# Optimization experiments

Hardware: AMD Instinct MI355X
Metric: run time of the kernel (lower is better)

## Reference

```python
import jax, jax.numpy as jnp
import numpy as np

GROUPS = 32
EPS = 1e-6

def group_norm(x, gamma, beta):
    b, c, h, w = x.shape
    xg = x.reshape(b, GROUPS, c // GROUPS, h, w)
    mu = jnp.mean(xg, axis=(2, 3, 4), keepdims=True)
    var = jnp.var(xg, axis=(2, 3, 4), keepdims=True)
    xn = ((xg - mu) * jax.lax.rsqrt(var + EPS)).reshape(b, c, h, w)
    return xn * gamma[None, :, None, None] + beta[None, :, None, None]

def conv1x1(x, w, b):
    # 1x1 conv == channel matmul: [B,C,H,W] x [O,C] -> [B,O,H,W]
    return jnp.einsum('bchw,oc->bohw', x, w) + b[None, :, None, None]

def setup_inputs() -> dict:
    key = jax.random.key(0)
    ks = jax.random.split(key, 5)
    B, C, H, W = 4, 512, 64, 64
    s = 1.0 / np.sqrt(C)
    return {
        'x': jax.random.normal(ks[0], (B, C, H, W), jnp.float32),
        'gn_gamma': jnp.ones((C,), jnp.float32),
        'gn_beta': jnp.zeros((C,), jnp.float32),
        'wq': jax.random.normal(ks[1], (C, C), jnp.float32) * s,
        'bq': jnp.zeros((C,), jnp.float32),
        'wk': jax.random.normal(ks[2], (C, C), jnp.float32) * s,
        'bk': jnp.zeros((C,), jnp.float32),
        'wv': jax.random.normal(ks[3], (C, C), jnp.float32) * s,
        'bv': jnp.zeros((C,), jnp.float32),
        'wp': jax.random.normal(ks[4], (C, C), jnp.float32) * s,
        'bp': jnp.zeros((C,), jnp.float32),
    }

def reference(x, gn_gamma, gn_beta, wq, bq, wk, bk, wv, bv, wp, bp):
    b, c, h, w = x.shape
    h_ = group_norm(x, gn_gamma, gn_beta)
    q = conv1x1(h_, wq, bq).reshape(b, c, h * w)  # [B,C,N]
    k = conv1x1(h_, wk, bk).reshape(b, c, h * w)
    v = conv1x1(h_, wv, bv).reshape(b, c, h * w)
    scale = jnp.asarray(c, x.dtype) ** -0.5
    # scores[b,i,j] = sum_c q[b,c,i] * k[b,c,j]
    scores = jnp.einsum('bci,bcj->bij', q, k) * scale
    attn = jax.nn.softmax(scores, axis=-1)  # softmax over keys j
    # out[b,c,i] = sum_j v[b,c,j] * attn[b,i,j]
    out = jnp.einsum('bcj,bij->bci', v, attn).reshape(b, c, h, w)
    out = conv1x1(out, wp, bp)
    return x + out
```

## Files before the change

### kernel.cpp

```cpp
#include <hip/hip_runtime.h>
#include <stdint.h>

#define B_N 4
#define C_N 512
#define SP_N 4096
#define NG 32
#define CPG 16
#define EPS_ 1e-6f

using bf16x8 = __attribute__((ext_vector_type(8))) __bf16;
using f32x4  = __attribute__((ext_vector_type(4))) float;

#define MFMA16(a, b, c) __builtin_amdgcn_mfma_f32_16x16x32_bf16(a, b, c, 0, 0, 0)

#define GLOAD16(gsrc, ldst) \
    __builtin_amdgcn_global_load_lds( \
        (const __attribute__((address_space(1))) unsigned int*)(gsrc), \
        (__attribute__((address_space(3))) unsigned int*)(ldst), 16, 0, 0)

__device__ __forceinline__ unsigned short f2bf(float f) {
    union { float f; unsigned u; } v; v.f = f;
    unsigned r = v.u + 0x7FFFu + ((v.u >> 16) & 1u);
    return (unsigned short)(r >> 16);
}
__device__ __forceinline__ float bf2f(unsigned short s) {
    union { unsigned u; float f; } v; v.u = ((unsigned)s) << 16;
    return v.f;
}

__global__ void wconv(const float* __restrict__ a, const float* __restrict__ b,
                      const float* __restrict__ c, const float* __restrict__ d,
                      unsigned short* __restrict__ dst) {
    int m = blockIdx.y;
    const float* src = m == 0 ? a : m == 1 ? b : m == 2 ? c : d;
    int i = blockIdx.x * 256 + threadIdx.x;
    float4 v = ((const float4*)src)[i];
    ushort4 o;
    o.x = f2bf(v.x); o.y = f2bf(v.y); o.z = f2bf(v.z); o.w = f2bf(v.w);
    ((ushort4*)(dst + (size_t)m * 262144))[i] = o;
}

__global__ __launch_bounds__(512) void gn_kernel(const float* __restrict__ x,
        const float* __restrict__ gamma, const float* __restrict__ beta,
        unsigned short* __restrict__ h_t) {
    int blk = blockIdx.x;
    int b = blk >> 5, g = blk & 31;
    const float* xg = x + ((size_t)(b * C_N + g * CPG)) * SP_N;
    int t = threadIdx.x;

    float s = 0.f, ss = 0.f;
    const float4* xv = (const float4*)xg;
    for (int i = t; i < (CPG * SP_N) / 4; i += 512) {
        float4 v = xv[i];
        s  += v.x + v.y + v.z + v.w;
        ss += v.x * v.x + v.y * v.y + v.z * v.z + v.w * v.w;
    }
    for (int m = 32; m; m >>= 1) { s += __shfl_xor(s, m); ss += __shfl_xor(ss, m); }
    __shared__ float rs[8], rss[8], stats[2];
    int wid = t >> 6;
    if ((t & 63) == 0) { rs[wid] = s; rss[wid] = ss; }
    __syncthreads();
    if (t == 0) {
        float a = 0.f, q = 0.f;
        for (int i = 0; i < 8; i++) { a += rs[i]; q += rss[i]; }
        float mean = a / (float)(CPG * SP_N);
        float var  = q / (float)(CPG * SP_N) - mean * mean;
        stats[0] = mean;
        stats[1] = rsqrtf(var + EPS_);
    }
    __shared__ float gam[CPG], bet[CPG];
    if (t < CPG) { gam[t] = gamma[g * CPG + t]; bet[t] = beta[g * CPG + t]; }
    __syncthreads();
    float mean = stats[0], rstd = stats[1];

    __shared__ unsigned short tile[CPG][130];
    unsigned short* hb = h_t + (size_t)b * SP_N * C_N;
    for (int n0 = 0; n0 < SP_N; n0 += 128) {
        __syncthreads();
#pragma unroll
        for (int p = 0; p < 4; p++) {
            int cc = p * 4 + (t >> 7);
            int nn = t & 127;
            float v = xg[(size_t)cc * SP_N + n0 + nn];
            v = (v - mean) * rstd * gam[cc] + bet[cc];
            tile[cc][nn] = f2bf(v);
        }
        __syncthreads();
#pragma unroll
        for (int p = 0; p < 4; p++) {
            int idx = p * 512 + t;
            int cc = idx & 15, nn = idx >> 4;
            hb[(size_t)(n0 + nn) * C_N + g * CPG + cc] = tile[cc][nn];
        }
    }
}

template<int MODE>
__global__ __launch_bounds__(256) void gemm_nt(
        const unsigned short* __restrict__ Ab,
        const unsigned short* __restrict__ Bb,
        void* __restrict__ outp,
        const float* __restrict__ bias,
        const float* __restrict__ resid,
        float qs) {
    __shared__ unsigned short at[128 * 64], bt[128 * 64];
    const int z = blockIdx.z;
    const size_t boff = (size_t)z * SP_N * C_N;
    const unsigned short* A;
    const unsigned short* Bm;
    int ldo;
    if (MODE <= 1) { A = Ab + boff; Bm = Bb; ldo = C_N; }
    else           { A = Ab;        Bm = Bb + boff; ldo = SP_N; }
    const int m0 = blockIdx.x * 128, n0 = blockIdx.y * 128;
    const int t = threadIdx.x;
    const int w = t >> 6, l = t & 63;
    const int wr = w >> 1, wc = w & 1;
    const int g = l >> 4, lr = l & 15;

    const f32x4 fz = {0.f, 0.f, 0.f, 0.f};
    f32x4 acc[4][4];
#pragma unroll
    for (int i = 0; i < 4; i++)
#pragma unroll
        for (int j = 0; j < 4; j++) acc[i][j] = fz;

    for (int k0 = 0; k0 < 512; k0 += 64) {
        __syncthreads();
#pragma unroll
        for (int r = 0; r < 4; r++) {
            int chunk = r * 256 + t;
            int row = chunk >> 3, ck = chunk & 7;
            uint4 da = *(const uint4*)(A + (size_t)(m0 + row) * 512 + k0 + ck * 8);
            *(uint4*)((char*)at + row * 128 + ((ck ^ (row & 7)) * 16)) = da;
            uint4 db = *(const uint4*)(Bm + (size_t)(n0 + row) * 512 + k0 + ck * 8);
            *(uint4*)((char*)bt + row * 128 + ((ck ^ (row & 7)) * 16)) = db;
        }
        __syncthreads();
#pragma unroll
        for (int ks = 0; ks < 2; ks++) {
            bf16x8 af[4], bfr[4];
#pragma unroll
            for (int mi = 0; mi < 4; mi++) {
                int row = wr * 64 + mi * 16 + lr;
                af[mi] = *(const bf16x8*)((const char*)at + row * 128 + (((ks * 4 + g) ^ (row & 7)) * 16));
            }
#pragma unroll
            for (int ni = 0; ni < 4; ni++) {
                int row = wc * 64 + ni * 16 + lr;
                bfr[ni] = *(const bf16x8*)((const char*)bt + row * 128 + (((ks * 4 + g) ^ (row & 7)) * 16));
            }
#pragma unroll
            for (int mi = 0; mi < 4; mi++)
#pragma unroll
                for (int ni = 0; ni < 4; ni++)
                    acc[mi][ni] = MFMA16(af[mi], bfr[ni], acc[mi][ni]);
        }
    }
#pragma unroll
    for (int mi = 0; mi < 4; mi++) {
#pragma unroll
        for (int ni = 0; ni < 4; ni++) {
            int col  = n0 + wc * 64 + ni * 16 + lr;
            int rowb = m0 + wr * 64 + mi * 16 + g * 4;
#pragma unroll
            for (int r = 0; r < 4; r++) {
                int row = rowb + r;
                float vv = acc[mi][ni][r];
                if (MODE == 0) {
                    size_t oi = boff + (size_t)row * ldo + col;
                    vv = (vv + bias[col]) * qs;
                    ((unsigned short*)outp)[oi] = f2bf(vv);
                } else if (MODE == 1) {
                    size_t oi = boff + (size_t)row * ldo + col;
                    vv += bias[col];
                    ((unsigned short*)outp)[oi] = f2bf(vv);
                } else if (MODE == 2) {
                    size_t oi = boff + (size_t)(col >> 5) * (C_N * 32) + row * 32 + (col & 31);
                    vv += bias[row];
                    ((unsigned short*)outp)[oi] = f2bf(vv);
                } else {
                    size_t oi = boff + (size_t)row * ldo + col;
                    vv += bias[row] + resid[oi];
                    ((float*)outp)[oi] = vv;
                }
            }
        }
    }
}

__global__ __launch_bounds__(256, 2) void attn_kernel(
        const unsigned short* __restrict__ qt,
        const unsigned short* __restrict__ kt,
        const unsigned short* __restrict__ vm,
        unsigned short* __restrict__ o0,
        unsigned short* __restrict__ o1,
        float* __restrict__ marr,
        float* __restrict__ larr) {
    __shared__ unsigned short k_lds[32 * 512];
    __shared__ unsigned short v_lds[512 * 40];
    __shared__ unsigned short p_lds[4][16 * 32];

    const int bid = blockIdx.x;
    const int bs = bid & 7;
    const int qtile = bid >> 3;
    const int b = bs >> 1;
    const int s = bs & 1;
    const int t = threadIdx.x;
    const int w = t >> 6;
    const int l = t & 63;
    const int g = l >> 4;
    const int lr = l & 15;

    unsigned short* outp = s == 0 ? o0 : o1;
    const int j_beg = s * (SP_N / 2);

    const unsigned short* qb = qt + ((size_t)b * SP_N + qtile * 64 + w * 16) * C_N;
    const unsigned short* kb = kt + (size_t)b * SP_N * C_N;
    const unsigned short* vb = vm + (size_t)b * SP_N * C_N;

    bf16x8 qf[16];
#pragma unroll
    for (int ks = 0; ks < 16; ks++)
        qf[ks] = *(const bf16x8*)(qb + (size_t)lr * C_N + ks * 32 + g * 8);

    const f32x4 fz = {0.f, 0.f, 0.f, 0.f};
    f32x4 oacc[32];
#pragma unroll
    for (int i = 0; i < 32; i++) oacc[i] = fz;
    f32x4 mst = {-1e30f, -1e30f, -1e30f, -1e30f};
    f32x4 lst = {0.f, 0.f, 0.f, 0.f};

    for (int j0 = j_beg; j0 < j_beg + SP_N / 2; j0 += 32) {
        __syncthreads();

#pragma unroll
        for (int r = 0; r < 8; r++) {
            int row = w * 8 + r;
            const unsigned short* src = kb + (size_t)(j0 + row) * C_N + (l ^ (row & 7)) * 8;
            GLOAD16(src, (char*)k_lds + row * 1024);
        }
        const unsigned short* vt = vb + (size_t)(j0 >> 5) * (C_N * 32);
        uint4 vdat[8];
#pragma unroll
        for (int r = 0; r < 8; r++) {
            int chunk = r * 256 + t;
            vdat[r] = *(const uint4*)(vt + (size_t)chunk * 8);
        }
#pragma unroll
        for (int r = 0; r < 8; r++) {
            int chunk = r * 256 + t;
            int c = chunk >> 2, jc = chunk & 3;
            *(uint4*)((char*)v_lds + c * 80 + jc * 16) = vdat[r];
        }
        __syncthreads();

        f32x4 s0 = fz, s1 = fz;
#pragma unroll
        for (int ks = 0; ks < 16; ks++) {
            bf16x8 kf0 = *(const bf16x8*)((const char*)k_lds + lr * 1024 + (((ks * 4 + g) ^ (lr & 7)) * 16));
            s0 = MFMA16(qf[ks], kf0, s0);
            int row1 = 16 + lr;
            bf16x8 kf1 = *(const bf16x8*)((const char*)k_lds + row1 * 1024 + (((ks * 4 + g) ^ (row1 & 7)) * 16));
            s1 = MFMA16(qf[ks], kf1, s1);
        }
        f32x4 mt;
#pragma unroll
        for (int r = 0; r < 4; r++) mt[r] = fmaxf(s0[r], s1[r]);
#pragma unroll
        for (int msk = 1; msk <= 8; msk <<= 1) {
#pragma unroll
            for (int r = 0; r < 4; r++) mt[r] = fmaxf(mt[r], __shfl_xor(mt[r], msk));
        }
        int inc = (mt[0] > mst[0]) || (mt[1] > mst[1]) || (mt[2] > mst[2]) || (mt[3] > mst[3]);
        if (__any(inc)) {
            f32x4 alpha;
#pragma unroll
            for (int r = 0; r < 4; r++) {
                float mn = fmaxf(mst[r], mt[r]);
                alpha[r] = exp2f(mst[r] - mn);
                mst[r] = mn;
                lst[r] *= alpha[r];
            }
            int src = (lr >> 2) << 4;
            float a0 = __shfl(alpha[0], src), a1 = __shfl(alpha[1], src);
            float a2 = __shfl(alpha[2], src), a3 = __shfl(alpha[3], src);
            int rr = lr & 3;
            float ac = rr == 0 ? a0 : rr == 1 ? a1 : rr == 2 ? a2 : a3;
#pragma unroll
            for (int i = 0; i < 32; i++) {
#pragma unroll
                for (int r = 0; r < 4; r++) oacc[i][r] *= ac;
            }
        }
        f32x4 p0, p1, rsum;
#pragma unroll
        for (int r = 0; r < 4; r++) {
            p0[r] = exp2f(s0[r] - mst[r]);
            p1[r] = exp2f(s1[r] - mst[r]);
            rsum[r] = p0[r] + p1[r];
        }
#pragma unroll
        for (int msk = 1; msk <= 8; msk <<= 1) {
#pragma unroll
            for (int r = 0; r < 4; r++) rsum[r] += __shfl_xor(rsum[r], msk);
        }
#pragma unroll
        for (int r = 0; r < 4; r++) lst[r] += rsum[r];

#pragma unroll
        for (int r = 0; r < 4; r++) {
            int i = g * 4 + r;
            int ja = lr;
            *(unsigned short*)((char*)p_lds[w] + i * 64 + (((ja >> 3) ^ ((i >> 1) & 3)) * 16) + (ja & 7) * 2) = f2bf(p0[r]);
            int jb = 16 + lr;
            *(unsigned short*)((char*)p_lds[w] + i * 64 + (((jb >> 3) ^ ((i >> 1) & 3)) * 16) + (jb & 7) * 2) = f2bf(p1[r]);
        }
        bf16x8 pf = *(const bf16x8*)((const char*)p_lds[w] + lr * 64 + ((g ^ ((lr >> 1) & 3)) * 16));
#pragma unroll
        for (int ct = 0; ct < 32; ct++) {
            int row = ct * 16 + lr;
            bf16x8 vf = *(const bf16x8*)((const char*)v_lds + row * 80 + g * 16);
            oacc[ct] = MFMA16(vf, pf, oacc[ct]);
        }
    }

    unsigned short* aob = outp + ((size_t)b * SP_N + qtile * 64 + w * 16 + lr) * C_N;
#pragma unroll
    for (int ct = 0; ct < 32; ct++) {
        int c0 = ct * 16 + g * 4;
        ushort4 o4;
        o4.x = f2bf(oacc[ct][0]);
        o4.y = f2bf(oacc[ct][1]);
        o4.z = f2bf(oacc[ct][2]);
        o4.w = f2bf(oacc[ct][3]);
        *(ushort4*)(aob + c0) = o4;
    }
    if (lr == 0) {
        int base = (s * B_N + b) * SP_N + qtile * 64 + w * 16 + g * 4;
#pragma unroll
        for (int r = 0; r < 4; r++) {
            marr[base + r] = mst[r];
            larr[base + r] = lst[r];
        }
    }
}

__global__ __launch_bounds__(256) void attn_combine(
        const unsigned short* __restrict__ o0,
        const unsigned short* __restrict__ o1,
        const float* __restrict__ marr,
        const float* __restrict__ larr,
        unsigned short* __restrict__ ao) {
    const int w = threadIdx.x >> 6, l = threadIdx.x & 63;
    const size_t row = (size_t)blockIdx.x * 4 + w;
    float m0 = marr[row], m1 = marr[B_N * SP_N + row];
    float l0 = larr[row], l1 = larr[B_N * SP_N + row];
    float m = fmaxf(m0, m1);
    float w0 = exp2f(m0 - m), w1 = exp2f(m1 - m);
    float den = w0 * l0 + w1 * l1;
    float a0 = w0 / den, a1 = w1 / den;
    uint4 u0 = *(const uint4*)(o0 + row * C_N + l * 8);
    uint4 u1 = *(const uint4*)(o1 + row * C_N + l * 8);
    const unsigned short* s0p = (const unsigned short*)&u0;
    const unsigned short* s1p = (const unsigned short*)&u1;
    unsigned short r8[8];
#pragma unroll
    for (int i = 0; i < 8; i++)
        r8[i] = f2bf(a0 * bf2f(s0p[i]) + a1 * bf2f(s1p[i]));
    *(uint4*)(ao + row * C_N + l * 8) = *(const uint4*)r8;
}

extern "C" void kernel_launch(void* const* d_in, const int* in_sizes, int n_in,
                              void* d_out, int out_size, void* d_ws, size_t ws_size,
                              hipStream_t stream) {
    const float* x   = (const float*)d_in[0];
    const float* gam = (const float*)d_in[1];
    const float* bet = (const float*)d_in[2];
    const float* wq  = (const float*)d_in[3];
    const float* bq  = (const float*)d_in[4];
    const float* wk  = (const float*)d_in[5];
    const float* bk  = (const float*)d_in[6];
    const float* wv  = (const float*)d_in[7];
    const float* bv  = (const float*)d_in[8];
    const float* wp  = (const float*)d_in[9];
    const float* bp  = (const float*)d_in[10];

    char* ws = (char*)d_ws;
    const size_t SZ = (size_t)B_N * SP_N * C_N * 2;
    unsigned short* h_t = (unsigned short*)(ws);
    unsigned short* q_t = (unsigned short*)(ws + SZ);
    unsigned short* k_t = (unsigned short*)(ws + 2 * SZ);
    unsigned short* v_m = (unsigned short*)(ws + 3 * SZ);
    unsigned short* wbf = (unsigned short*)(ws + 4 * SZ);
    unsigned short* wq_b = wbf;
    unsigned short* wk_b = wbf + 262144;
    unsigned short* wv_b = wbf + 2 * 262144;
    unsigned short* wp_b = wbf + 3 * 262144;
    float* marr = (float*)(ws + 4 * SZ + 4 * 524288);
    float* larr = marr + 2 * B_N * SP_N;

    unsigned short* o0 = h_t;
    unsigned short* o1 = (unsigned short*)d_out;
    unsigned short* ao = q_t;

    const float qs = 0.044194173824159216f * 1.4426950408889634f;

    wconv<<<dim3(256, 4), 256, 0, stream>>>(wq, wk, wv, wp, wbf);
    gn_kernel<<<dim3(128), 512, 0, stream>>>(x, gam, bet, h_t);
    gemm_nt<0><<<dim3(32, 4, 4), 256, 0, stream>>>(h_t, wq_b, q_t, bq, nullptr, qs);
    gemm_nt<1><<<dim3(32, 4, 4), 256, 0, stream>>>(h_t, wk_b, k_t, bk, nullptr, 1.f);
    gemm_nt<2><<<dim3(4, 32, 4), 256, 0, stream>>>(wv_b, h_t, v_m, bv, nullptr, 1.f);
    attn_kernel<<<dim3(512), 256, 0, stream>>>(q_t, k_t, v_m, o0, o1, marr, larr);
    attn_combine<<<dim3(B_N * SP_N / 4), 256, 0, stream>>>(o0, o1, marr, larr, ao);
    gemm_nt<3><<<dim3(4, 32, 4), 256, 0, stream>>>(wp_b, ao, d_out, bp, x, 1.f);
}
```

Before: 703.4 us.

## Split attention keys three ways and read V directly from global memory

The key range is now split into three parts instead of two, so the grid has 768 blocks and a third partial output buffer. The combine kernel merges three partial softmax states. V is no longer staged through shared memory; each lane loads its V fragments straight from global memory. Dropping the V tile frees LDS, which lets the launch bound ask for 3 blocks per CU. The trade-off is uncached, uncoalesced-per-MFMA global V reads and extra combine traffic.

```diff
diff --git a/kernel.cpp b/kernel.cpp
--- a/kernel.cpp
+++ b/kernel.cpp
@@ -7,6 +7,7 @@
 #define NG 32
 #define CPG 16
 #define EPS_ 1e-6f
+#define NSPLIT 3
 
 using bf16x8 = __attribute__((ext_vector_type(8))) __bf16;
 using f32x4  = __attribute__((ext_vector_type(4))) float;
@@ -188,31 +189,32 @@
     }
 }
 
-__global__ __launch_bounds__(256, 2) void attn_kernel(
+__global__ __launch_bounds__(256, 3) void attn_kernel(
         const unsigned short* __restrict__ qt,
         const unsigned short* __restrict__ kt,
         const unsigned short* __restrict__ vm,
         unsigned short* __restrict__ o0,
         unsigned short* __restrict__ o1,
+        unsigned short* __restrict__ o2,
         float* __restrict__ marr,
         float* __restrict__ larr) {
     __shared__ unsigned short k_lds[32 * 512];
-    __shared__ unsigned short v_lds[512 * 40];
     __shared__ unsigned short p_lds[4][16 * 32];
 
     const int bid = blockIdx.x;
-    const int bs = bid & 7;
-    const int qtile = bid >> 3;
-    const int b = bs >> 1;
-    const int s = bs & 1;
+    const int sb = bid % 12;
+    const int qtile = bid / 12;
+    const int b = sb & 3;
+    const int s = sb >> 2;
     const int t = threadIdx.x;
     const int w = t >> 6;
     const int l = t & 63;
     const int g = l >> 4;
     const int lr = l & 15;
 
-    unsigned short* outp = s == 0 ? o0 : o1;
-    const int j_beg = s * (SP_N / 2);
+    unsigned short* outp = s == 0 ? o0 : (s == 1 ? o1 : o2);
+    const int jt_beg = s * 43;
+    const int jt_end = (s == 2) ? 128 : (s + 1) * 43;
 
     const unsigned short* qb = qt + ((size_t)b * SP_N + qtile * 64 + w * 16) * C_N;
     const unsigned short* kb = kt + (size_t)b * SP_N * C_N;
@@ -230,7 +232,8 @@
     f32x4 mst = {-1e30f, -1e30f, -1e30f, -1e30f};
     f32x4 lst = {0.f, 0.f, 0.f, 0.f};
 
-    for (int j0 = j_beg; j0 < j_beg + SP_N / 2; j0 += 32) {
+    for (int jt = jt_beg; jt < jt_end; jt++) {
+        const int j0 = jt * 32;
         __syncthreads();
 
 #pragma unroll
@@ -238,19 +241,6 @@
             int row = w * 8 + r;
             const unsigned short* src = kb + (size_t)(j0 + row) * C_N + (l ^ (row & 7)) * 8;
             GLOAD16(src, (char*)k_lds + row * 1024);
-        }
-        const unsigned short* vt = vb + (size_t)(j0 >> 5) * (C_N * 32);
-        uint4 vdat[8];
-#pragma unroll
-        for (int r = 0; r < 8; r++) {
-            int chunk = r * 256 + t;
-            vdat[r] = *(const uint4*)(vt + (size_t)chunk * 8);
-        }
-#pragma unroll
-        for (int r = 0; r < 8; r++) {
-            int chunk = r * 256 + t;
-            int c = chunk >> 2, jc = chunk & 3;
-            *(uint4*)((char*)v_lds + c * 80 + jc * 16) = vdat[r];
         }
         __syncthreads();
 
@@ -316,10 +306,11 @@
             *(unsigned short*)((char*)p_lds[w] + i * 64 + (((jb >> 3) ^ ((i >> 1) & 3)) * 16) + (jb & 7) * 2) = f2bf(p1[r]);
         }
         bf16x8 pf = *(const bf16x8*)((const char*)p_lds[w] + lr * 64 + ((g ^ ((lr >> 1) & 3)) * 16));
+
+        const unsigned short* vt = vb + (size_t)jt * (C_N * 32);
 #pragma unroll
         for (int ct = 0; ct < 32; ct++) {
-            int row = ct * 16 + lr;
-            bf16x8 vf = *(const bf16x8*)((const char*)v_lds + row * 80 + g * 16);
+            bf16x8 vf = *(const bf16x8*)(vt + (ct * 16 + lr) * 32 + g * 8);
             oacc[ct] = MFMA16(vf, pf, oacc[ct]);
         }
     }
@@ -348,25 +339,28 @@
 __global__ __launch_bounds__(256) void attn_combine(
         const unsigned short* __restrict__ o0,
         const unsigned short* __restrict__ o1,
+        const unsigned short* __restrict__ o2,
         const float* __restrict__ marr,
         const float* __restrict__ larr,
         unsigned short* __restrict__ ao) {
     const int w = threadIdx.x >> 6, l = threadIdx.x & 63;
     const size_t row = (size_t)blockIdx.x * 4 + w;
-    float m0 = marr[row], m1 = marr[B_N * SP_N + row];
-    float l0 = larr[row], l1 = larr[B_N * SP_N + row];
-    float m = fmaxf(m0, m1);
-    float w0 = exp2f(m0 - m), w1 = exp2f(m1 - m);
-    float den = w0 * l0 + w1 * l1;
-    float a0 = w0 / den, a1 = w1 / den;
+    float m0 = marr[row], m1 = marr[B_N * SP_N + row], m2 = marr[2 * B_N * SP_N + row];
+    float l0 = larr[row], l1 = larr[B_N * SP_N + row], l2 = larr[2 * B_N * SP_N + row];
+    float m = fmaxf(fmaxf(m0, m1), m2);
+    float w0 = exp2f(m0 - m), w1 = exp2f(m1 - m), w2 = exp2f(m2 - m);
+    float den = w0 * l0 + w1 * l1 + w2 * l2;
+    float a0 = w0 / den, a1 = w1 / den, a2 = w2 / den;
     uint4 u0 = *(const uint4*)(o0 + row * C_N + l * 8);
     uint4 u1 = *(const uint4*)(o1 + row * C_N + l * 8);
+    uint4 u2 = *(const uint4*)(o2 + row * C_N + l * 8);
     const unsigned short* s0p = (const unsigned short*)&u0;
     const unsigned short* s1p = (const unsigned short*)&u1;
+    const unsigned short* s2p = (const unsigned short*)&u2;
     unsigned short r8[8];
 #pragma unroll
     for (int i = 0; i < 8; i++)
-        r8[i] = f2bf(a0 * bf2f(s0p[i]) + a1 * bf2f(s1p[i]));
+        r8[i] = f2bf(a0 * bf2f(s0p[i]) + a1 * bf2f(s1p[i]) + a2 * bf2f(s2p[i]));
     *(uint4*)(ao + row * C_N + l * 8) = *(const uint4*)r8;
 }
 
@@ -397,10 +391,11 @@
     unsigned short* wv_b = wbf + 2 * 262144;
     unsigned short* wp_b = wbf + 3 * 262144;
     float* marr = (float*)(ws + 4 * SZ + 4 * 524288);
-    float* larr = marr + 2 * B_N * SP_N;
+    float* larr = marr + NSPLIT * B_N * SP_N;
 
     unsigned short* o0 = h_t;
     unsigned short* o1 = (unsigned short*)d_out;
+    unsigned short* o2 = (unsigned short*)d_out + (size_t)B_N * SP_N * C_N;
     unsigned short* ao = q_t;
 
     const float qs = 0.044194173824159216f * 1.4426950408889634f;
@@ -410,7 +405,7 @@
     gemm_nt<0><<<dim3(32, 4, 4), 256, 0, stream>>>(h_t, wq_b, q_t, bq, nullptr, qs);
     gemm_nt<1><<<dim3(32, 4, 4), 256, 0, stream>>>(h_t, wk_b, k_t, bk, nullptr, 1.f);
     gemm_nt<2><<<dim3(4, 32, 4), 256, 0, stream>>>(wv_b, h_t, v_m, bv, nullptr, 1.f);
-    attn_kernel<<<dim3(512), 256, 0, stream>>>(q_t, k_t, v_m, o0, o1, marr, larr);
-    attn_combine<<<dim3(B_N * SP_N / 4), 256, 0, stream>>>(o0, o1, marr, larr, ao);
+    attn_kernel<<<dim3(768), 256, 0, stream>>>(q_t, k_t, v_m, o0, o1, o2, marr, larr);
+    attn_combine<<<dim3(B_N * SP_N / 4), 256, 0, stream>>>(o0, o1, o2, marr, larr, ao);
     gemm_nt<3><<<dim3(4, 32, 4), 256, 0, stream>>>(wp_b, ao, d_out, bp, x, 1.f);
 }
```

New measurement: 1.186 ms. 1.69x slower.

## Process two query sub-tiles per wave in attention to reuse K/V LDS loads

Applied to the files above, without the earlier changes.

Each wave now handles 32 query rows (two 16-row sub-tiles) instead of 16, so each K and V tile staged in LDS feeds twice as many MFMAs. The grid is halved to 256 blocks and launch bounds drop to one block per CU to make room for the doubled accumulators and Q fragments. The V staging load is also split into two halves to limit live registers. The trade-off is fewer waves in flight, so less latency hiding, and only 256 blocks, which may underfill the GPU's compute units.

```diff
diff --git a/kernel.cpp b/kernel.cpp
--- a/kernel.cpp
+++ b/kernel.cpp
@@ -188,7 +188,7 @@
     }
 }
 
-__global__ __launch_bounds__(256, 2) void attn_kernel(
+__global__ __launch_bounds__(256, 1) void attn_kernel(
         const unsigned short* __restrict__ qt,
         const unsigned short* __restrict__ kt,
         const unsigned short* __restrict__ vm,
@@ -198,7 +198,7 @@
         float* __restrict__ larr) {
     __shared__ unsigned short k_lds[32 * 512];
     __shared__ unsigned short v_lds[512 * 40];
-    __shared__ unsigned short p_lds[4][16 * 32];
+    __shared__ unsigned short p_lds[4][2][16 * 32];
 
     const int bid = blockIdx.x;
     const int bs = bid & 7;
@@ -214,21 +214,25 @@
     unsigned short* outp = s == 0 ? o0 : o1;
     const int j_beg = s * (SP_N / 2);
 
-    const unsigned short* qb = qt + ((size_t)b * SP_N + qtile * 64 + w * 16) * C_N;
+    const unsigned short* qb = qt + ((size_t)b * SP_N + qtile * 128 + w * 32) * C_N;
     const unsigned short* kb = kt + (size_t)b * SP_N * C_N;
     const unsigned short* vb = vm + (size_t)b * SP_N * C_N;
 
-    bf16x8 qf[16];
-#pragma unroll
-    for (int ks = 0; ks < 16; ks++)
-        qf[ks] = *(const bf16x8*)(qb + (size_t)lr * C_N + ks * 32 + g * 8);
+    bf16x8 qf[2][16];
+#pragma unroll
+    for (int sub = 0; sub < 2; sub++)
+#pragma unroll
+        for (int ks = 0; ks < 16; ks++)
+            qf[sub][ks] = *(const bf16x8*)(qb + (size_t)(sub * 16 + lr) * C_N + ks * 32 + g * 8);
 
     const f32x4 fz = {0.f, 0.f, 0.f, 0.f};
-    f32x4 oacc[32];
-#pragma unroll
-    for (int i = 0; i < 32; i++) oacc[i] = fz;
-    f32x4 mst = {-1e30f, -1e30f, -1e30f, -1e30f};
-    f32x4 lst = {0.f, 0.f, 0.f, 0.f};
+    f32x4 oacc[2][32];
+#pragma unroll
+    for (int sub = 0; sub < 2; sub++)
+#pragma unroll
+        for (int i = 0; i < 32; i++) oacc[sub][i] = fz;
+    f32x4 mst[2] = {{-1e30f, -1e30f, -1e30f, -1e30f}, {-1e30f, -1e30f, -1e30f, -1e30f}};
+    f32x4 lst[2] = {fz, fz};
 
     for (int j0 = j_beg; j0 < j_beg + SP_N / 2; j0 += 32) {
         __syncthreads();
@@ -240,107 +244,128 @@
             GLOAD16(src, (char*)k_lds + row * 1024);
         }
         const unsigned short* vt = vb + (size_t)(j0 >> 5) * (C_N * 32);
-        uint4 vdat[8];
-#pragma unroll
-        for (int r = 0; r < 8; r++) {
-            int chunk = r * 256 + t;
-            vdat[r] = *(const uint4*)(vt + (size_t)chunk * 8);
-        }
-#pragma unroll
-        for (int r = 0; r < 8; r++) {
-            int chunk = r * 256 + t;
-            int c = chunk >> 2, jc = chunk & 3;
-            *(uint4*)((char*)v_lds + c * 80 + jc * 16) = vdat[r];
-        }
-        __syncthreads();
-
-        f32x4 s0 = fz, s1 = fz;
+        {
+            uint4 vdat[4];
+#pragma unroll
+            for (int r = 0; r < 4; r++) vdat[r] = *(const uint4*)(vt + (size_t)(r * 256 + t) * 8);
+#pragma unroll
+            for (int r = 0; r < 4; r++) {
+                int chunk = r * 256 + t;
+                *(uint4*)((char*)v_lds + (chunk >> 2) * 80 + (chunk & 3) * 16) = vdat[r];
+            }
+#pragma unroll
+            for (int r = 0; r < 4; r++) vdat[r] = *(const uint4*)(vt + (size_t)((r + 4) * 256 + t) * 8);
+#pragma unroll
+            for (int r = 0; r < 4; r++) {
+                int chunk = (r + 4) * 256 + t;
+                *(uint4*)((char*)v_lds + (chunk >> 2) * 80 + (chunk & 3) * 16) = vdat[r];
+            }
+        }
+        __syncthreads();
+
+        f32x4 s00 = fz, s01 = fz, s10 = fz, s11 = fz;
 #pragma unroll
         for (int ks = 0; ks < 16; ks++) {
             bf16x8 kf0 = *(const bf16x8*)((const char*)k_lds + lr * 1024 + (((ks * 4 + g) ^ (lr & 7)) * 16));
-            s0 = MFMA16(qf[ks], kf0, s0);
             int row1 = 16 + lr;
             bf16x8 kf1 = *(const bf16x8*)((const char*)k_lds + row1 * 1024 + (((ks * 4 + g) ^ (row1 & 7)) * 16));
-            s1 = MFMA16(qf[ks], kf1, s1);
-        }
-        f32x4 mt;
-#pragma unroll
-        for (int r = 0; r < 4; r++) mt[r] = fmaxf(s0[r], s1[r]);
-#pragma unroll
-        for (int msk = 1; msk <= 8; msk <<= 1) {
-#pragma unroll
-            for (int r = 0; r < 4; r++) mt[r] = fmaxf(mt[r], __shfl_xor(mt[r], msk));
-        }
-        int inc = (mt[0] > mst[0]) || (mt[1] > mst[1]) || (mt[2] > mst[2]) || (mt[3] > mst[3]);
-        if (__any(inc)) {
-            f32x4 alpha;
-#pragma unroll
-            for (int r = 0; r < 4; r++) {
-                float mn = fmaxf(mst[r], mt[r]);
-                alpha[r] = exp2f(mst[r] - mn);
-                mst[r] = mn;
-                lst[r] *= alpha[r];
-            }
-            int src = (lr >> 2) << 4;
-            float a0 = __shfl(alpha[0], src), a1 = __shfl(alpha[1], src);
-            float a2 = __shfl(alpha[2], src), a3 = __shfl(alpha[3], src);
-            int rr = lr & 3;
-            float ac = rr == 0 ? a0 : rr == 1 ? a1 : rr == 2 ? a2 : a3;
-#pragma unroll
-            for (int i = 0; i < 32; i++) {
-#pragma unroll
-                for (int r = 0; r < 4; r++) oacc[i][r] *= ac;
-            }
-        }
-        f32x4 p0, p1, rsum;
-#pragma unroll
-        for (int r = 0; r < 4; r++) {
-            p0[r] = exp2f(s0[r] - mst[r]);
-            p1[r] = exp2f(s1[r] - mst[r]);
-            rsum[r] = p0[r] + p1[r];
-        }
-#pragma unroll
-        for (int msk = 1; msk <= 8; msk <<= 1) {
-#pragma unroll
-            for (int r = 0; r < 4; r++) rsum[r] += __shfl_xor(rsum[r], msk);
-        }
-#pragma unroll
-        for (int r = 0; r < 4; r++) lst[r] += rsum[r];
-
-#pragma unroll
-        for (int r = 0; r < 4; r++) {
-            int i = g * 4 + r;
-            int ja = lr;
-            *(unsigned short*)((char*)p_lds[w] + i * 64 + (((ja >> 3) ^ ((i >> 1) & 3)) * 16) + (ja & 7) * 2) = f2bf(p0[r]);
-            int jb = 16 + lr;
-            *(unsigned short*)((char*)p_lds[w] + i * 64 + (((jb >> 3) ^ ((i >> 1) & 3)) * 16) + (jb & 7) * 2) = f2bf(p1[r]);
-        }
-        bf16x8 pf = *(const bf16x8*)((const char*)p_lds[w] + lr * 64 + ((g ^ ((lr >> 1) & 3)) * 16));
+            s00 = MFMA16(qf[0][ks], kf0, s00);
+            s01 = MFMA16(qf[0][ks], kf1, s01);
+            s10 = MFMA16(qf[1][ks], kf0, s10);
+            s11 = MFMA16(qf[1][ks], kf1, s11);
+        }
+
+        bf16x8 pf[2];
+#pragma unroll
+        for (int sub = 0; sub < 2; sub++) {
+            f32x4 sA = sub == 0 ? s00 : s10;
+            f32x4 sB = sub == 0 ? s01 : s11;
+            f32x4 mt;
+#pragma unroll
+            for (int r = 0; r < 4; r++) mt[r] = fmaxf(sA[r], sB[r]);
+#pragma unroll
+            for (int msk = 1; msk <= 8; msk <<= 1) {
+#pragma unroll
+                for (int r = 0; r < 4; r++) mt[r] = fmaxf(mt[r], __shfl_xor(mt[r], msk));
+            }
+            int inc = (mt[0] > mst[sub][0]) || (mt[1] > mst[sub][1]) ||
+                      (mt[2] > mst[sub][2]) || (mt[3] > mst[sub][3]);
+            if (__any(inc)) {
+                f32x4 alpha;
+#pragma unroll
+                for (int r = 0; r < 4; r++) {
+                    float mn = fmaxf(mst[sub][r], mt[r]);
+                    alpha[r] = exp2f(mst[sub][r] - mn);
+                    mst[sub][r] = mn;
+                    lst[sub][r] *= alpha[r];
+                }
+                int src = (lr >> 2) << 4;
+                float a0 = __shfl(alpha[0], src), a1 = __shfl(alpha[1], src);
+                float a2 = __shfl(alpha[2], src), a3 = __shfl(alpha[3], src);
+                int rr = lr & 3;
+                float ac = rr == 0 ? a0 : rr == 1 ? a1 : rr == 2 ? a2 : a3;
+#pragma unroll
+                for (int i = 0; i < 32; i++) {
+#pragma unroll
+                    for (int r = 0; r < 4; r++) oacc[sub][i][r] *= ac;
+                }
+            }
+            f32x4 p0, p1, rsum;
+#pragma unroll
+            for (int r = 0; r < 4; r++) {
+                p0[r] = exp2f(sA[r] - mst[sub][r]);
+                p1[r] = exp2f(sB[r] - mst[sub][r]);
+                rsum[r] = p0[r] + p1[r];
+            }
+#pragma unroll
+            for (int msk = 1; msk <= 8; msk <<= 1) {
+#pragma unroll
+                for (int r = 0; r < 4; r++) rsum[r] += __shfl_xor(rsum[r], msk);
+            }
+#pragma unroll
+            for (int r = 0; r < 4; r++) lst[sub][r] += rsum[r];
+
+            char* pb = (char*)p_lds + (w * 2 + sub) * 1024;
+#pragma unroll
+            for (int r = 0; r < 4; r++) {
+                int i = g * 4 + r;
+                int ja = lr;
+                *(unsigned short*)(pb + i * 64 + (((ja >> 3) ^ ((i >> 1) & 3)) * 16) + (ja & 7) * 2) = f2bf(p0[r]);
+                int jb = 16 + lr;
+                *(unsigned short*)(pb + i * 64 + (((jb >> 3) ^ ((i >> 1) & 3)) * 16) + (jb & 7) * 2) = f2bf(p1[r]);
+            }
+            pf[sub] = *(const bf16x8*)(pb + lr * 64 + ((g ^ ((lr >> 1) & 3)) * 16));
+        }
+
 #pragma unroll
         for (int ct = 0; ct < 32; ct++) {
             int row = ct * 16 + lr;
             bf16x8 vf = *(const bf16x8*)((const char*)v_lds + row * 80 + g * 16);
-            oacc[ct] = MFMA16(vf, pf, oacc[ct]);
-        }
-    }
-
-    unsigned short* aob = outp + ((size_t)b * SP_N + qtile * 64 + w * 16 + lr) * C_N;
-#pragma unroll
-    for (int ct = 0; ct < 32; ct++) {
-        int c0 = ct * 16 + g * 4;
-        ushort4 o4;
-        o4.x = f2bf(oacc[ct][0]);
-        o4.y = f2bf(oacc[ct][1]);
-        o4.z = f2bf(oacc[ct][2]);
-        o4.w = f2bf(oacc[ct][3]);
-        *(ushort4*)(aob + c0) = o4;
-    }
-    if (lr == 0) {
-        int base = (s * B_N + b) * SP_N + qtile * 64 + w * 16 + g * 4;
-#pragma unroll
-        for (int r = 0; r < 4; r++) {
-            marr[base + r] = mst[r];
-            larr[base + r] = lst[r];
+            oacc[0][ct] = MFMA16(vf, pf[0], oacc[0][ct]);
+            oacc[1][ct] = MFMA16(vf, pf[1], oacc[1][ct]);
+        }
+    }
+
+#pragma unroll
+    for (int sub = 0; sub < 2; sub++) {
+        unsigned short* aob = outp + ((size_t)b * SP_N + qtile * 128 + w * 32 + sub * 16 + lr) * C_N;
+#pragma unroll
+        for (int ct = 0; ct < 32; ct++) {
+            int c0 = ct * 16 + g * 4;
+            ushort4 o4;
+            o4.x = f2bf(oacc[sub][ct][0]);
+            o4.y = f2bf(oacc[sub][ct][1]);
+            o4.z = f2bf(oacc[sub][ct][2]);
+            o4.w = f2bf(oacc[sub][ct][3]);
+            *(ushort4*)(aob + c0) = o4;
+        }
+        if (lr == 0) {
+            int base = (s * B_N + b) * SP_N + qtile * 128 + w * 32 + sub * 16 + g * 4;
+#pragma unroll
+            for (int r = 0; r < 4; r++) {
+                marr[base + r] = mst[sub][r];
+                larr[base + r] = lst[sub][r];
+            }
         }
     }
 }
@@ -410,7 +435,7 @@
     gemm_nt<0><<<dim3(32, 4, 4), 256, 0, stream>>>(h_t, wq_b, q_t, bq, nullptr, qs);
     gemm_nt<1><<<dim3(32, 4, 4), 256, 0, stream>>>(h_t, wk_b, k_t, bk, nullptr, 1.f);
     gemm_nt<2><<<dim3(4, 32, 4), 256, 0, stream>>>(wv_b, h_t, v_m, bv, nullptr, 1.f);
-    attn_kernel<<<dim3(512), 256, 0, stream>>>(q_t, k_t, v_m, o0, o1, marr, larr);
+    attn_kernel<<<dim3(256), 256, 0, stream>>>(q_t, k_t, v_m, o0, o1, marr, larr);
     attn_combine<<<dim3(B_N * SP_N / 4), 256, 0, stream>>>(o0, o1, marr, larr, ao);
     gemm_nt<3><<<dim3(4, 32, 4), 256, 0, stream>>>(wp_b, ao, d_out, bp, x, 1.f);
 }
```

Measured after the change: 1.776 ms. 2.52x slower.
